# Performance work log

Hardware: AMD Instinct MI355X
Metric: run time of the kernel (lower is better)

Reference implementation:

```python
import jax, jax.numpy as jnp
import numpy as np

B, N, P, E, H, D, F, L = 16, 500, 100, 128, 8, 16, 512, 6
CLIP = 10.0  # logit_clipping


def _heads(x, h):
    b, n, _ = x.shape
    return x.reshape(b, n, h, -1).transpose(0, 2, 1, 3)  # [b,h,n,d]


def _mha(q, k, v, mask3=None):
    d = q.shape[-1]
    s = jnp.einsum('bhnd,bhmd->bhnm', q, k) / jnp.sqrt(jnp.asarray(d, q.dtype))
    if mask3 is not None:
        s = s + mask3[:, None, :, :]
    w = jax.nn.softmax(s, axis=-1)
    o = jnp.einsum('bhnm,bhmd->bhnd', w, v)
    b, h, n, dd = o.shape
    return o.transpose(0, 2, 1, 3).reshape(b, n, h * dd)


def _ff(x, w1, b1, w2, b2):
    return jax.nn.relu(x @ w1 + b1) @ w2 + b2


def _forward(depot_xy, node_xy, node_demand, load, cur_dist, ninf_mask,
             emb_depot_w, emb_depot_b, emb_node_w, emb_node_b,
             enc_wq, enc_wk, enc_wv, enc_comb_w, enc_comb_b,
             enc_ff1_w, enc_ff1_b, enc_ff2_w, enc_ff2_b,
             dec_wq_last, dec_wk, dec_wv, dec_comb_w, dec_comb_b,
             dec_cap_w, dec_ff1_w, dec_ff1_b, dec_ff2_w, dec_ff2_b,
             current_node):
    # ---------------- encoder ----------------
    node_xy_demand = jnp.concatenate([node_xy, node_demand[:, :, None]], axis=2)  # [B,N,3]
    x = jnp.concatenate([depot_xy @ emb_depot_w + emb_depot_b,
                         node_xy_demand @ emb_node_w + emb_node_b], axis=1)  # [B,N+1,E]
    for i in range(L):
        q = _heads(x @ enc_wq[i], H)
        k = _heads(x @ enc_wk[i], H)
        v = _heads(x @ enc_wv[i], H)
        mh = _mha(q, k, v) @ enc_comb_w[i] + enc_comb_b[i]
        o1 = x + mh
        x = o1 + _ff(o1, enc_ff1_w[i], enc_ff1_b[i], enc_ff2_w[i], enc_ff2_b[i])
    encoded_nodes = x  # [B, N+1, E]
    # decoder kv cache (set_kv)
    k = _heads(encoded_nodes @ dec_wk, H)
    v = _heads(encoded_nodes @ dec_wv, H)
    # ---------------- one decode step ----------------
    encoded_last = jnp.take_along_axis(encoded_nodes, current_node[:, :, None], axis=1)  # [B,P,E]
    input_cat = jnp.concatenate([encoded_last, load[:, :, None]], axis=2)  # [B,P,E+1]
    q = _heads(input_cat @ dec_wq_last, H)
    mh = _mha(q, k, v, mask3=ninf_mask) @ dec_comb_w + dec_comb_b
    mh = mh + encoded_last + load[:, :, None] @ dec_cap_w
    q_ref = _ff(mh, dec_ff1_w, dec_ff1_b, dec_ff2_w, dec_ff2_b) + mh
    score = jnp.einsum('bpe,bne->bpn', q_ref, encoded_nodes) / jnp.sqrt(jnp.asarray(E, q_ref.dtype))
    # distance-based noise injection
    dmin = cur_dist.min(axis=-1, keepdims=True)
    dmax = cur_dist.max(axis=-1, keepdims=True)
    norm_dist = (cur_dist - dmin) / (dmax - dmin + 1e-6)
    problem_size = ninf_mask.shape[2]
    nm = 50.0 / problem_size
    base_noise = jax.random.normal(jax.random.key(42), cur_dist.shape, cur_dist.dtype) * 0.2 + 0.5
    score = score - (1.0 - nm) * jnp.log(norm_dist + 1e-6) + base_noise * nm
    score = CLIP * jnp.tanh(score) + ninf_mask
    return jax.nn.softmax(score, axis=2)  # [B,P,N+1]


def setup_inputs() -> dict:
    key = jax.random.key(0)
    ks = iter(jax.random.split(key, 40))
    def rn(shape, s=0.02):
        return s * jax.random.normal(next(ks), shape, jnp.float32)
    return dict(
        depot_xy=jax.random.uniform(next(ks), (B, 1, 2), jnp.float32),
        node_xy=jax.random.uniform(next(ks), (B, N, 2), jnp.float32),
        node_demand=jax.random.uniform(next(ks), (B, N), jnp.float32),
        load=jax.random.uniform(next(ks), (B, P), jnp.float32),
        cur_dist=jax.random.uniform(next(ks), (B, P, N + 1), jnp.float32),
        ninf_mask=jnp.zeros((B, P, N + 1), jnp.float32),
        current_node=jax.random.randint(next(ks), (B, P), 0, N + 1),
        emb_depot_w=rn((2, E)), emb_depot_b=rn((E,)),
        emb_node_w=rn((3, E)), emb_node_b=rn((E,)),
        enc_wq=rn((L, E, H * D)), enc_wk=rn((L, E, H * D)), enc_wv=rn((L, E, H * D)),
        enc_comb_w=rn((L, H * D, E)), enc_comb_b=rn((L, E)),
        enc_ff1_w=rn((L, E, F)), enc_ff1_b=rn((L, F)),
        enc_ff2_w=rn((L, F, E)), enc_ff2_b=rn((L, E)),
        dec_wq_last=rn((E + 1, H * D)), dec_wk=rn((E, H * D)), dec_wv=rn((E, H * D)),
        dec_comb_w=rn((H * D, E)), dec_comb_b=rn((E,)),
        dec_cap_w=rn((1, E)),
        dec_ff1_w=rn((E, F)), dec_ff1_b=rn((F,)),
        dec_ff2_w=rn((F, E)), dec_ff2_b=rn((E,)),
    )


def reference(depot_xy, node_xy, node_demand, load, cur_dist, ninf_mask, current_node,
              emb_depot_w, emb_depot_b, emb_node_w, emb_node_b,
              enc_wq, enc_wk, enc_wv, enc_comb_w, enc_comb_b,
              enc_ff1_w, enc_ff1_b, enc_ff2_w, enc_ff2_b,
              dec_wq_last, dec_wk, dec_wv, dec_comb_w, dec_comb_b,
              dec_cap_w, dec_ff1_w, dec_ff1_b, dec_ff2_w, dec_ff2_b):
    return _forward(depot_xy, node_xy, node_demand, load, cur_dist, ninf_mask,
                    emb_depot_w, emb_depot_b, emb_node_w, emb_node_b,
                    enc_wq, enc_wk, enc_wv, enc_comb_w, enc_comb_b,
                    enc_ff1_w, enc_ff1_b, enc_ff2_w, enc_ff2_b,
                    dec_wq_last, dec_wk, dec_wv, dec_comb_w, dec_comb_b,
                    dec_cap_w, dec_ff1_w, dec_ff1_b, dec_ff2_w, dec_ff2_b,
                    current_node)
```

## Files before the change

### kernel.cpp

```cpp
#include <hip/hip_runtime.h>
#include <math.h>

#define Bb 16
#define Nn 500
#define NT 501
#define Pp 100
#define Ee 128
#define Hh 8
#define Dd 16
#define Ff 512
#define Ll 6
#define Mtok (Bb*NT)
#define PR (Bb*Pp)
#define TJ 32
#define SPLIT 4
#define KSEG 126
#define DSPLIT 4
#define DSEG 126
#define ENCP (6*128*384)
#define DECP (128*256)
#define SNP 512

__global__ __launch_bounds__(256) void pack_k(
    const float* __restrict__ ewq, const float* __restrict__ ewk, const float* __restrict__ ewv,
    const float* __restrict__ dwk, const float* __restrict__ dwv,
    float* __restrict__ encP, float* __restrict__ decP)
{
  int i = blockIdx.x*256 + threadIdx.x;
  if (i < ENCP) {
    int l = i / (128*384); int rem = i - l*128*384; int k = rem / 384; int n = rem - k*384;
    float v;
    if (n < 128)      v = ewq[((size_t)l*128 + k)*128 + n];
    else if (n < 256) v = ewk[((size_t)l*128 + k)*128 + (n-128)];
    else              v = ewv[((size_t)l*128 + k)*128 + (n-256)];
    encP[i] = v;
  } else {
    int j = i - ENCP;
    if (j < DECP) {
      int k = j >> 8; int n = j & 255;
      decP[j] = (n < 128) ? dwk[k*128 + n] : dwv[k*128 + (n-128)];
    }
  }
}

__global__ __launch_bounds__(256) void embed_k(
    const float* __restrict__ depot_xy, const float* __restrict__ node_xy,
    const float* __restrict__ node_demand,
    const float* __restrict__ wD, const float* __restrict__ bD,
    const float* __restrict__ wN, const float* __restrict__ bN,
    float* __restrict__ x)
{
  int t = blockIdx.x*256 + threadIdx.x;
  if (t >= Mtok*Ee) return;
  int e   = t & (Ee-1);
  int tok = t >> 7;
  int b   = tok / NT;
  int n   = tok - b*NT;
  float v;
  if (n == 0) {
    v = depot_xy[b*2+0]*wD[0*Ee+e] + depot_xy[b*2+1]*wD[1*Ee+e] + bD[e];
  } else {
    int nn = n - 1;
    float c0 = node_xy[(b*Nn + nn)*2 + 0];
    float c1 = node_xy[(b*Nn + nn)*2 + 1];
    float c2 = node_demand[b*Nn + nn];
    v = c0*wN[0*Ee+e] + c1*wN[1*Ee+e] + c2*wN[2*Ee+e] + bN[e];
  }
  x[(size_t)tok*Ee + e] = v;
}

__global__ __launch_bounds__(256) void gemm_k(
    const float* __restrict__ A, const float* __restrict__ W,
    const float* __restrict__ bias, const float* __restrict__ res,
    float* __restrict__ C, int M, int N, int K, int relu)
{
  __shared__ __align__(16) float As[2][16][68];
  __shared__ __align__(16) float Bs[2][16][68];
  int tid = threadIdx.x;
  int tx = tid & 15, ty = tid >> 4;
  int m0 = blockIdx.x * 64, n0 = blockIdx.y * 64;
  float acc[4][4];
  #pragma unroll
  for (int i=0;i<4;i++)
    #pragma unroll
    for (int j=0;j<4;j++) acc[i][j] = 0.f;

  int ar = tid >> 2;
  int ak = (tid & 3) << 2;
  int br = tid >> 4;
  int bc = (tid & 15) << 2;

  const float* Ap = A + (size_t)(m0 + ar)*K + ak;
  const float* Wp = W + (size_t)br*N + n0 + bc;
  bool aok = (m0 + ar) < M;

  float4 av = aok ? *(const float4*)(Ap) : make_float4(0.f,0.f,0.f,0.f);
  float4 wv = *(const float4*)(Wp);

  int nk = K >> 4;
  for (int t = 0; t < nk; ++t) {
    int cur = t & 1;
    As[cur][ak+0][ar] = av.x; As[cur][ak+1][ar] = av.y;
    As[cur][ak+2][ar] = av.z; As[cur][ak+3][ar] = av.w;
    *(float4*)(&Bs[cur][br][bc]) = wv;
    __syncthreads();
    if (t+1 < nk) {
      av = aok ? *(const float4*)(Ap + (t+1)*16) : make_float4(0.f,0.f,0.f,0.f);
      wv = *(const float4*)(Wp + (size_t)(t+1)*16*N);
    }
    #pragma unroll
    for (int k=0;k<16;k++){
      float4 a4 = *(const float4*)(&As[cur][k][ty*4]);
      float4 b4 = *(const float4*)(&Bs[cur][k][tx*4]);
      float avv[4] = {a4.x,a4.y,a4.z,a4.w};
      float bvv[4] = {b4.x,b4.y,b4.z,b4.w};
      #pragma unroll
      for (int i=0;i<4;i++)
        #pragma unroll
        for (int j=0;j<4;j++)
          acc[i][j] = fmaf(avv[i], bvv[j], acc[i][j]);
    }
  }

  float4 bv = make_float4(0.f,0.f,0.f,0.f);
  if (bias) bv = *(const float4*)(bias + n0 + tx*4);
  #pragma unroll
  for (int i=0;i<4;i++){
    int row = m0 + ty*4 + i;
    if (row >= M) continue;
    float4 o;
    o.x = acc[i][0] + bv.x; o.y = acc[i][1] + bv.y;
    o.z = acc[i][2] + bv.z; o.w = acc[i][3] + bv.w;
    if (relu){ o.x=fmaxf(o.x,0.f); o.y=fmaxf(o.y,0.f); o.z=fmaxf(o.z,0.f); o.w=fmaxf(o.w,0.f); }
    if (res){
      float4 rv = *(const float4*)(res + (size_t)row*N + n0 + tx*4);
      o.x += rv.x; o.y += rv.y; o.z += rv.z; o.w += rv.w;
    }
    *(float4*)(C + (size_t)row*N + n0 + tx*4) = o;
  }
}

__device__ __forceinline__ float dot4(float4 a, float4 b){
  return fmaf(a.x,b.x, fmaf(a.y,b.y, fmaf(a.z,b.z, a.w*b.w)));
}

__global__ __launch_bounds__(256) void attn_enc_k(
    const float* __restrict__ QKV, float* __restrict__ part_o,
    float* __restrict__ part_l)
{
  int blk = blockIdx.x;
  int s  = blk % SPLIT;
  int cc = blk / SPLIT;
  int c  = cc & 1;
  int bh = cc >> 1;
  int h  = bh & (Hh-1);
  int b  = bh >> 3;
  int p  = c*256 + (int)threadIdx.x;
  const int klo = s*KSEG;
  int kseg = NT - klo; if (kseg > KSEG) kseg = KSEG;

  __shared__ __align__(16) float4 Ks[2][TJ][4];
  __shared__ __align__(16) float4 Vs[2][TJ][4];

  int tid = threadIdx.x;
  int row = (tid >> 2) & 31;
  int lc  = tid & 3;
  bool isV = tid >= 128;
  const int kvoff = isV ? 256 : 128;

  float4 q0,q1,q2,q3;
  if (p < NT) {
    const float4* qp = (const float4*)(QKV + ((size_t)(b*NT + p))*384 + h*Dd);
    q0=qp[0]; q1=qp[1]; q2=qp[2]; q3=qp[3];
  } else {
    q0=q1=q2=q3=make_float4(0,0,0,0);
  }

  if (row < kseg) {
    float4 v = *((const float4*)(QKV + ((size_t)(b*NT + klo + row))*384 + kvoff + h*Dd) + lc);
    if (isV) Vs[0][row][lc] = v; else Ks[0][row][lc] = v;
  }
  __syncthreads();

  float l = 0.f;
  float4 o0=make_float4(0,0,0,0), o1=o0, o2=o0, o3=o0;
  const int ntiles = (kseg + TJ - 1)/TJ;
  int buf = 0;

  for (int t = 0; t < ntiles; ++t) {
    int j0 = t*TJ;
    if (t+1 < ntiles) {
      int jj = j0 + TJ + row;
      if (jj < kseg) {
        float4 v = *((const float4*)(QKV + ((size_t)(b*NT + klo + jj))*384 + kvoff + h*Dd) + lc);
        if (isV) Vs[buf^1][row][lc] = v; else Ks[buf^1][row][lc] = v;
      }
    }
    int jend = kseg - j0; if (jend > TJ) jend = TJ;

    if (p < NT) {
      #pragma unroll 4
      for (int jj=0;jj<jend;jj++){
        const float4* kr = &Ks[buf][jj][0];
        float s0 = (dot4(q0,kr[0])+dot4(q1,kr[1])) + (dot4(q2,kr[2])+dot4(q3,kr[3]));
        float w = __expf(s0 * 0.25f);
        l += w;
        const float4* vr = &Vs[buf][jj][0];
        float4 v0=vr[0],v1=vr[1],v2=vr[2],v3=vr[3];
        o0.x=fmaf(w,v0.x,o0.x); o0.y=fmaf(w,v0.y,o0.y); o0.z=fmaf(w,v0.z,o0.z); o0.w=fmaf(w,v0.w,o0.w);
        o1.x=fmaf(w,v1.x,o1.x); o1.y=fmaf(w,v1.y,o1.y); o1.z=fmaf(w,v1.z,o1.z); o1.w=fmaf(w,v1.w,o1.w);
        o2.x=fmaf(w,v2.x,o2.x); o2.y=fmaf(w,v2.y,o2.y); o2.z=fmaf(w,v2.z,o2.z); o2.w=fmaf(w,v2.w,o2.w);
        o3.x=fmaf(w,v3.x,o3.x); o3.y=fmaf(w,v3.y,o3.y); o3.z=fmaf(w,v3.z,o3.z); o3.w=fmaf(w,v3.w,o3.w);
      }
    }
    __syncthreads();
    buf ^= 1;
  }

  if (p < NT) {
    size_t rbase = ((size_t)s*128 + bh)*NT + p;
    float4* po = (float4*)(part_o + rbase*16);
    po[0]=o0; po[1]=o1; po[2]=o2; po[3]=o3;
    part_l[rbase] = l;
  }
}

__global__ __launch_bounds__(256) void attn_comb_k(
    const float* __restrict__ part_o, const float* __restrict__ part_l,
    float* __restrict__ O)
{
  int t = blockIdx.x*256 + threadIdx.x;
  if (t >= 128*NT*16) return;
  int d  = t & 15;
  int rq = t >> 4;
  int q  = rq % NT;
  int bh = rq / NT;
  int h = bh & 7, b = bh >> 3;
  const size_t R = (size_t)128*NT;
  float L = 0.f, o = 0.f;
  #pragma unroll
  for (int s=0;s<SPLIT;s++){
    L += part_l[(size_t)s*R + rq];
    o += part_o[((size_t)s*R + rq)*16 + d];
  }
  O[((size_t)(b*NT + q))*Ee + h*Dd + d] = o / L;
}

__global__ __launch_bounds__(128) void attn_dec_k(
    const float* __restrict__ Q, const float* __restrict__ KV,
    const float* __restrict__ mask,
    float* __restrict__ part_o, float* __restrict__ part_l)
{
  int blk = blockIdx.x;
  int s  = blk & (DSPLIT-1);
  int bh = blk >> 2;
  int h  = bh & (Hh-1);
  int b  = bh >> 3;
  int klo = s*DSEG;
  int kn  = NT - klo; if (kn > DSEG) kn = DSEG;

  __shared__ __align__(16) float4 Ks[DSEG][4];
  __shared__ __align__(16) float4 Vs[DSEG][4];

  int tid = threadIdx.x;
  for (int i = tid; i < kn*8; i += 128) {
    int row  = i >> 3;
    int q8   = i & 7;
    int quad = q8 & 3;
    int isv  = q8 >> 2;
    float4 v = *(const float4*)(KV + ((size_t)(b*NT + klo + row))*256 + isv*128 + h*Dd + quad*4);
    if (isv) Vs[row][quad] = v; else Ks[row][quad] = v;
  }
  __syncthreads();

  int p = tid;
  if (p >= Pp) return;
  int r = b*Pp + p;
  const float4* qp = (const float4*)(Q + (size_t)r*Ee + h*Dd);
  float4 qa=qp[0], qb=qp[1], qc=qp[2], qd=qp[3];
  const float* mrow = mask + (size_t)r*NT + klo;

  float l = 0.f;
  float4 o0=make_float4(0,0,0,0), o1=o0, o2=o0, o3=o0;
  for (int j=0;j<kn;++j){
    float sc = (dot4(qa,Ks[j][0])+dot4(qb,Ks[j][1])) + (dot4(qc,Ks[j][2])+dot4(qd,Ks[j][3]));
    float w = __expf(sc*0.25f + mrow[j]);
    l += w;
    float4 v0=Vs[j][0],v1=Vs[j][1],v2=Vs[j][2],v3=Vs[j][3];
    o0.x=fmaf(w,v0.x,o0.x); o0.y=fmaf(w,v0.y,o0.y); o0.z=fmaf(w,v0.z,o0.z); o0.w=fmaf(w,v0.w,o0.w);
    o1.x=fmaf(w,v1.x,o1.x); o1.y=fmaf(w,v1.y,o1.y); o1.z=fmaf(w,v1.z,o1.z); o1.w=fmaf(w,v1.w,o1.w);
    o2.x=fmaf(w,v2.x,o2.x); o2.y=fmaf(w,v2.y,o2.y); o2.z=fmaf(w,v2.z,o2.z); o2.w=fmaf(w,v2.w,o2.w);
    o3.x=fmaf(w,v3.x,o3.x); o3.y=fmaf(w,v3.y,o3.y); o3.z=fmaf(w,v3.z,o3.z); o3.w=fmaf(w,v3.w,o3.w);
  }

  size_t rb = ((size_t)s*PR + r)*Hh + h;
  float4* po = (float4*)(part_o + rb*16);
  po[0]=o0; po[1]=o1; po[2]=o2; po[3]=o3;
  part_l[rb] = l;
}

__global__ __launch_bounds__(256) void attn_dcomb_k(
    const float* __restrict__ part_o, const float* __restrict__ part_l,
    float* __restrict__ O)
{
  int t = blockIdx.x*256 + threadIdx.x;
  if (t >= PR*Ee) return;
  int d = t & 15;
  int h = (t >> 4) & 7;
  int r = t >> 7;
  const size_t S = (size_t)PR*Hh;
  size_t rb = (size_t)r*Hh + h;
  float L = 0.f, o = 0.f;
  #pragma unroll
  for (int s=0;s<DSPLIT;s++){
    L += part_l[(size_t)s*S + rb];
    o += part_o[((size_t)s*S + rb)*16 + d];
  }
  O[(size_t)r*Ee + h*Dd + d] = o / L;
}

__global__ __launch_bounds__(256) void gather_k(
    const float* __restrict__ x, const int* __restrict__ cur, float* __restrict__ encl)
{
  int t = blockIdx.x*256 + threadIdx.x;
  if (t >= PR*Ee) return;
  int e = t & (Ee-1);
  int r = t >> 7;
  int b = r / Pp;
  int node = cur[r];
  encl[(size_t)r*Ee + e] = x[((size_t)(b*NT + node))*Ee + e];
}

__global__ __launch_bounds__(128) void decq_k(
    const float* __restrict__ encl, const float* __restrict__ loadv,
    const float* __restrict__ Wq, float* __restrict__ q)
{
  __shared__ float row[Ee];
  int r = blockIdx.x, e = threadIdx.x;
  row[e] = encl[(size_t)r*Ee + e];
  __syncthreads();
  float acc = 0.f;
  #pragma unroll 4
  for (int k=0;k<Ee;k++) acc = fmaf(row[k], Wq[k*128 + e], acc);
  acc = fmaf(loadv[r], Wq[Ee*128 + e], acc);
  q[(size_t)r*128 + e] = acc;
}

__global__ __launch_bounds__(128) void dec_comb_k(
    const float* __restrict__ att, const float* __restrict__ W,
    const float* __restrict__ bias, const float* __restrict__ encl,
    const float* __restrict__ loadv, const float* __restrict__ capw,
    float* __restrict__ mh)
{
  __shared__ float row[Ee];
  int r = blockIdx.x, e = threadIdx.x;
  row[e] = att[(size_t)r*Ee + e];
  __syncthreads();
  float acc = 0.f;
  #pragma unroll 4
  for (int k=0;k<Ee;k++) acc = fmaf(row[k], W[k*Ee + e], acc);
  mh[(size_t)r*Ee + e] = acc + bias[e] + encl[(size_t)r*Ee + e] + loadv[r]*capw[e];
}

__global__ __launch_bounds__(256) void xt_k(
    const float* __restrict__ x, float* __restrict__ xT)
{
  __shared__ float T[32][33];
  int n0 = blockIdx.x * 32;
  int k0 = blockIdx.y * 32;
  int b  = blockIdx.z;
  int t  = threadIdx.x;
  int row = t >> 3;
  int c4  = (t & 7) << 2;

  int n = n0 + row;
  float4 v = make_float4(0.f,0.f,0.f,0.f);
  if (n < NT) v = *(const float4*)(x + ((size_t)(b*NT + n))*Ee + k0 + c4);
  T[c4+0][row] = v.x; T[c4+1][row] = v.y; T[c4+2][row] = v.z; T[c4+3][row] = v.w;
  __syncthreads();

  const float SC = 0.08838834764831845f;
  float4 o;
  o.x = T[row][c4+0]*SC; o.y = T[row][c4+1]*SC;
  o.z = T[row][c4+2]*SC; o.w = T[row][c4+3]*SC;
  *(float4*)(xT + ((size_t)(b*Ee + k0 + row))*SNP + n0 + c4) = o;
}

__global__ __launch_bounds__(256) void score_gemm_k(
    const float* __restrict__ qref, const float* __restrict__ xT,
    float* __restrict__ score)
{
  __shared__ __align__(16) float As[2][16][68];
  __shared__ __align__(16) float Bs[2][16][68];
  int tid = threadIdx.x;
  int tx = tid & 15, ty = tid >> 4;
  int m0 = blockIdx.x * 64;
  int n0 = blockIdx.y * 64;
  int b  = blockIdx.z;

  const float* A = qref + (size_t)b*Pp*Ee;
  const float* W = xT   + (size_t)b*Ee*SNP;
  float*       C = score + (size_t)b*Pp*SNP;

  float acc[4][4];
  #pragma unroll
  for (int i=0;i<4;i++)
    #pragma unroll
    for (int j=0;j<4;j++) acc[i][j] = 0.f;

  int ar = tid >> 2;
  int ak = (tid & 3) << 2;
  int br = tid >> 4;
  int bc = (tid & 15) << 2;

  const float* Ap = A + (size_t)(m0 + ar)*Ee + ak;
  const float* Wp = W + (size_t)br*SNP + n0 + bc;
  bool aok = (m0 + ar) < Pp;

  float4 av = aok ? *(const float4*)(Ap) : make_float4(0.f,0.f,0.f,0.f);
  float4 wv = *(const float4*)(Wp);

  for (int t = 0; t < 8; ++t) {
    int cur = t & 1;
    As[cur][ak+0][ar] = av.x; As[cur][ak+1][ar] = av.y;
    As[cur][ak+2][ar] = av.z; As[cur][ak+3][ar] = av.w;
    *(float4*)(&Bs[cur][br][bc]) = wv;
    __syncthreads();
    if (t+1 < 8) {
      av = aok ? *(const float4*)(Ap + (t+1)*16) : make_float4(0.f,0.f,0.f,0.f);
      wv = *(const float4*)(Wp + (size_t)(t+1)*16*SNP);
    }
    #pragma unroll
    for (int k=0;k<16;k++){
      float4 a4 = *(const float4*)(&As[cur][k][ty*4]);
      float4 b4 = *(const float4*)(&Bs[cur][k][tx*4]);
      float avv[4] = {a4.x,a4.y,a4.z,a4.w};
      float bvv[4] = {b4.x,b4.y,b4.z,b4.w};
      #pragma unroll
      for (int i=0;i<4;i++)
        #pragma unroll
        for (int j=0;j<4;j++)
          acc[i][j] = fmaf(avv[i], bvv[j], acc[i][j]);
    }
    __syncthreads();
  }

  #pragma unroll
  for (int i=0;i<4;i++){
    int row = m0 + ty*4 + i;
    if (row >= Pp) continue;
    float4 o;
    o.x = acc[i][0]; o.y = acc[i][1]; o.z = acc[i][2]; o.w = acc[i][3];
    *(float4*)(C + (size_t)row*SNP + n0 + tx*4) = o;
  }
}

__device__ __forceinline__ unsigned rotl32(unsigned x, int r){ return (x<<r)|(x>>(32-r)); }

__device__ float tf_normal(unsigned idx)
{
  unsigned x0 = 0u;
  unsigned x1 = idx;
  const unsigned ks[3] = {0u, 42u, 0u ^ 42u ^ 0x1BD11BDAu};
  x0 += ks[0]; x1 += ks[1];
  const int rotA[4] = {13,15,26,6};
  const int rotB[4] = {17,29,16,24};
  #pragma unroll
  for (int i=0;i<5;i++){
    #pragma unroll
    for (int q=0;q<4;q++){
      int rr = (i&1) ? rotB[q] : rotA[q];
      x0 += x1; x1 = rotl32(x1, rr); x1 ^= x0;
    }
    x0 += ks[(i+1)%3];
    x1 += ks[(i+2)%3] + (unsigned)(i+1);
  }
  unsigned bits = x0 ^ x1;
  float f = __uint_as_float((bits >> 9) | 0x3f800000u) - 1.0f;
  const float lo = -0.99999994f;
  float u = f * 2.0f + lo;
  u = fmaxf(lo, u);
  float w = -log1pf(-u*u);
  float p;
  if (w < 5.0f) {
    w -= 2.5f;
    p = 2.81022636e-08f;
    p = fmaf(p, w, 3.43273939e-07f);
    p = fmaf(p, w, -3.5233877e-06f);
    p = fmaf(p, w, -4.39150654e-06f);
    p = fmaf(p, w, 0.00021858087f);
    p = fmaf(p, w, -0.00125372503f);
    p = fmaf(p, w, -0.00417768164f);
    p = fmaf(p, w, 0.246640727f);
    p = fmaf(p, w, 1.50140941f);
  } else {
    w = sqrtf(w) - 3.0f;
    p = -0.000200214257f;
    p = fmaf(p, w, 0.000100950558f);
    p = fmaf(p, w, 0.00134934322f);
    p = fmaf(p, w, -0.00367342844f);
    p = fmaf(p, w, 0.00573950773f);
    p = fmaf(p, w, -0.0076224613f);
    p = fmaf(p, w, 0.00943887047f);
    p = fmaf(p, w, 1.00167406f);
    p = fmaf(p, w, 2.83297682f);
  }
  return 1.4142135623730951f * (p * u);
}

__global__ __launch_bounds__(512) void final_k(
    const float* __restrict__ score, const float* __restrict__ cur_dist,
    const float* __restrict__ ninf, float* __restrict__ out)
{
  __shared__ float smn[8], smx[8], sm2[8], ss[8];
  const float NM = (float)(50.0/501.0);
  const float C1 = (float)(1.0 - 50.0/501.0);
  int r = blockIdx.x;
  int t = threadIdx.x;
  int wid = t >> 6, lane = t & 63;

  float cd = 0.f;
  float mn = 1e30f, mx = -1e30f;
  if (t < NT) { cd = cur_dist[(size_t)r*NT + t]; mn = cd; mx = cd; }
  #pragma unroll
  for (int off=32; off>=1; off>>=1){
    mn = fminf(mn, __shfl_xor(mn, off));
    mx = fmaxf(mx, __shfl_xor(mx, off));
  }
  if (lane == 0){ smn[wid] = mn; smx[wid] = mx; }
  __syncthreads();
  float dmin = smn[0], dmax = smx[0];
  #pragma unroll
  for (int i=1;i<8;i++){ dmin = fminf(dmin, smn[i]); dmax = fmaxf(dmax, smx[i]); }

  float sval = -1e30f;
  if (t < NT) {
    float nd = (cd - dmin) / (dmax - dmin + 1e-6f);
    float z  = tf_normal((unsigned)r*501u + (unsigned)t);
    float s  = score[(size_t)r*SNP + t] - C1*logf(nd + 1e-6f) + (z*0.2f + 0.5f)*NM;
    sval = 10.0f*tanhf(s) + ninf[(size_t)r*NT + t];
  }
  float mv = sval;
  #pragma unroll
  for (int off=32; off>=1; off>>=1) mv = fmaxf(mv, __shfl_xor(mv, off));
  if (lane == 0) sm2[wid] = mv;
  __syncthreads();
  float smax = sm2[0];
  #pragma unroll
  for (int i=1;i<8;i++) smax = fmaxf(smax, sm2[i]);

  float e = (t < NT) ? expf(sval - smax) : 0.f;
  float sv = e;
  #pragma unroll
  for (int off=32; off>=1; off>>=1) sv += __shfl_xor(sv, off);
  if (lane == 0) ss[wid] = sv;
  __syncthreads();
  float ssum = ss[0];
  #pragma unroll
  for (int i=1;i<8;i++) ssum += ss[i];

  if (t < NT) out[(size_t)r*NT + t] = e / ssum;
}

extern "C" void kernel_launch(void* const* d_in, const int* in_sizes, int n_in,
                              void* d_out, int out_size, void* d_ws, size_t ws_size,
                              hipStream_t stream)
{
  (void)in_sizes; (void)n_in; (void)out_size; (void)ws_size;
  const float* depot_xy    = (const float*)d_in[0];
  const float* node_xy     = (const float*)d_in[1];
  const float* node_demand = (const float*)d_in[2];
  const float* loadv       = (const float*)d_in[3];
  const float* cur_dist    = (const float*)d_in[4];
  const float* ninf        = (const float*)d_in[5];
  const int*   cur_node    = (const int*)d_in[6];
  const float* emb_depot_w = (const float*)d_in[7];
  const float* emb_depot_b = (const float*)d_in[8];
  const float* emb_node_w  = (const float*)d_in[9];
  const float* emb_node_b  = (const float*)d_in[10];
  const float* enc_wq      = (const float*)d_in[11];
  const float* enc_wk      = (const float*)d_in[12];
  const float* enc_wv      = (const float*)d_in[13];
  const float* enc_comb_w  = (const float*)d_in[14];
  const float* enc_comb_b  = (const float*)d_in[15];
  const float* enc_ff1_w   = (const float*)d_in[16];
  const float* enc_ff1_b   = (const float*)d_in[17];
  const float* enc_ff2_w   = (const float*)d_in[18];
  const float* enc_ff2_b   = (const float*)d_in[19];
  const float* dec_wq_last = (const float*)d_in[20];
  const float* dec_wk      = (const float*)d_in[21];
  const float* dec_wv      = (const float*)d_in[22];
  const float* dec_comb_w  = (const float*)d_in[23];
  const float* dec_comb_b  = (const float*)d_in[24];
  const float* dec_cap_w   = (const float*)d_in[25];
  const float* dec_ff1_w   = (const float*)d_in[26];
  const float* dec_ff1_b   = (const float*)d_in[27];
  const float* dec_ff2_w   = (const float*)d_in[28];
  const float* dec_ff2_b   = (const float*)d_in[29];

  float* ws = (float*)d_ws;
  const size_t SZ = (size_t)Mtok*Ee;
  float* xb    = ws + 0*SZ;
  float* qkvb  = ws + 1*SZ;
  float* atb   = ws + 4*SZ;
  float* o1b   = ws + 5*SZ;
  float* ffb   = ws + 6*SZ;
  float* encPk = ws + 10*SZ;
  float* decPk = encPk + ENCP;
  float* part_o = ffb;
  float* part_l = o1b;
  float* dpart_o = ffb;
  float* dpart_l = o1b;
  float* encl  = qkvb + 2*SZ;
  float* qdec  = encl + 204800;
  float* attd  = qdec + 204800;
  float* mhb   = attd + 204800;
  float* qrefb = atb;
  float* ffh2  = ffb;
  float* xTb   = ffb;
  float* scoreb= o1b;

  pack_k<<<(ENCP + DECP + 255)/256, 256, 0, stream>>>(
      enc_wq, enc_wk, enc_wv, dec_wk, dec_wv, encPk, decPk);

  embed_k<<<(Mtok*Ee + 255)/256, 256, 0, stream>>>(
      depot_xy, node_xy, node_demand, emb_depot_w, emb_depot_b,
      emb_node_w, emb_node_b, xb);

  dim3 gqkv((Mtok + 63)/64, 384/64);
  dim3 g128((Mtok + 63)/64, Ee/64);
  dim3 gff ((Mtok + 63)/64, Ff/64);
  const int gcomb = (128*NT*16 + 255)/256;
  for (int l = 0; l < Ll; ++l) {
    gemm_k<<<gqkv, 256, 0, stream>>>(xb, encPk + (size_t)l*128*384, nullptr, nullptr, qkvb, Mtok, 384, Ee, 0);
    attn_enc_k<<<Bb*Hh*2*SPLIT, 256, 0, stream>>>(qkvb, part_o, part_l);
    attn_comb_k<<<gcomb, 256, 0, stream>>>(part_o, part_l, atb);
    gemm_k<<<g128, 256, 0, stream>>>(atb, enc_comb_w + (size_t)l*Ee*Ee, enc_comb_b + l*Ee, xb, o1b, Mtok, Ee, Ee, 0);
    gemm_k<<<gff, 256, 0, stream>>>(o1b, enc_ff1_w + (size_t)l*Ee*Ff, enc_ff1_b + l*Ff, nullptr, ffb, Mtok, Ff, Ee, 1);
    gemm_k<<<g128, 256, 0, stream>>>(ffb, enc_ff2_w + (size_t)l*Ff*Ee, enc_ff2_b + l*Ee, o1b, xb, Mtok, Ee, Ff, 0);
  }

  dim3 gkv((Mtok + 63)/64, 256/64);
  gemm_k<<<gkv, 256, 0, stream>>>(xb, decPk, nullptr, nullptr, qkvb, Mtok, 256, Ee, 0);
  gather_k<<<(PR*Ee + 255)/256, 256, 0, stream>>>(xb, cur_node, encl);
  decq_k<<<PR, 128, 0, stream>>>(encl, loadv, dec_wq_last, qdec);
  attn_dec_k<<<Bb*Hh*DSPLIT, 128, 0, stream>>>(qdec, qkvb, ninf, dpart_o, dpart_l);
  attn_dcomb_k<<<(PR*Ee + 255)/256, 256, 0, stream>>>(dpart_o, dpart_l, attd);
  dec_comb_k<<<PR, 128, 0, stream>>>(attd, dec_comb_w, dec_comb_b, encl, loadv, dec_cap_w, mhb);
  dim3 gd1((PR + 63)/64, Ff/64);
  gemm_k<<<gd1, 256, 0, stream>>>(mhb, dec_ff1_w, dec_ff1_b, nullptr, ffh2, PR, Ff, Ee, 1);
  dim3 gd2((PR + 63)/64, Ee/64);
  gemm_k<<<gd2, 256, 0, stream>>>(ffh2, dec_ff2_w, dec_ff2_b, mhb, qrefb, PR, Ee, Ff, 0);
  dim3 gxt(16, 4, 16);
  xt_k<<<gxt, 256, 0, stream>>>(xb, xTb);
  dim3 gsc(2, 8, 16);
  score_gemm_k<<<gsc, 256, 0, stream>>>(qrefb, xTb, scoreb);
  final_k<<<PR, 512, 0, stream>>>(scoreb, cur_dist, ninf, (float*)d_out);
}
```

Before: 909.5 us.

## Fuse attention split-combine into projection GEMMs and retile attention kernels

The encoder split-K attention combine is folded into the output-projection GEMM, which reads the partial sums directly, and the attention kernel now uses 128 threads that each handle two queries so K/V loads from shared memory are reused. In the decoder, the gather is merged into the query projection and the partial combine into the comb-projection kernel. The decoder split count also goes from 4 to 16 for more parallelism. This removes several launches and intermediate round trips, at the cost of redundant partial reads inside the GEMM and more registers in the attention kernel.

```diff
diff --git a/kernel.cpp b/kernel.cpp
--- a/kernel.cpp
+++ b/kernel.cpp
@@ -15,8 +15,8 @@
 #define TJ 32
 #define SPLIT 4
 #define KSEG 126
-#define DSPLIT 4
-#define DSEG 126
+#define DSPLIT 16
+#define DSEG 32
 #define ENCP (6*128*384)
 #define DECP (128*256)
 #define SNP 512
@@ -144,7 +144,7 @@
   return fmaf(a.x,b.x, fmaf(a.y,b.y, fmaf(a.z,b.z, a.w*b.w)));
 }
 
-__global__ __launch_bounds__(256) void attn_enc_k(
+__global__ __launch_bounds__(128) void attn_enc_k(
     const float* __restrict__ QKV, float* __restrict__ part_o,
     float* __restrict__ part_l)
 {
@@ -155,95 +155,172 @@
   int bh = cc >> 1;
   int h  = bh & (Hh-1);
   int b  = bh >> 3;
-  int p  = c*256 + (int)threadIdx.x;
+  int tid = threadIdx.x;
+  int p0 = c*256 + tid;
+  int p1 = p0 + 128;
   const int klo = s*KSEG;
   int kseg = NT - klo; if (kseg > KSEG) kseg = KSEG;
 
   __shared__ __align__(16) float4 Ks[2][TJ][4];
   __shared__ __align__(16) float4 Vs[2][TJ][4];
 
-  int tid = threadIdx.x;
-  int row = (tid >> 2) & 31;
-  int lc  = tid & 3;
-  bool isV = tid >= 128;
-  const int kvoff = isV ? 256 : 128;
-
-  float4 q0,q1,q2,q3;
-  if (p < NT) {
-    const float4* qp = (const float4*)(QKV + ((size_t)(b*NT + p))*384 + h*Dd);
-    q0=qp[0]; q1=qp[1]; q2=qp[2]; q3=qp[3];
+  bool vbq = p1 < NT;
+
+  const float4* qp = (const float4*)(QKV + ((size_t)(b*NT + p0))*384 + h*Dd);
+  float4 qa0=qp[0], qa1=qp[1], qa2=qp[2], qa3=qp[3];
+  float4 qb0,qb1,qb2,qb3;
+  if (vbq) {
+    const float4* q2 = (const float4*)(QKV + ((size_t)(b*NT + p1))*384 + h*Dd);
+    qb0=q2[0]; qb1=q2[1]; qb2=q2[2]; qb3=q2[3];
   } else {
-    q0=q1=q2=q3=make_float4(0,0,0,0);
-  }
-
-  if (row < kseg) {
-    float4 v = *((const float4*)(QKV + ((size_t)(b*NT + klo + row))*384 + kvoff + h*Dd) + lc);
-    if (isV) Vs[0][row][lc] = v; else Ks[0][row][lc] = v;
+    qb0=qb1=qb2=qb3=make_float4(0,0,0,0);
+  }
+
+  {
+    int rows = kseg < TJ ? kseg : TJ;
+    for (int i = tid; i < rows*8; i += 128) {
+      int row = i >> 3; int q8 = i & 7; int quad = q8 & 3; int isv = q8 >> 2;
+      float4 v = *(const float4*)(QKV + ((size_t)(b*NT + klo + row))*384 + (isv ? 256 : 128) + h*Dd + quad*4);
+      if (isv) Vs[0][row][quad] = v; else Ks[0][row][quad] = v;
+    }
   }
   __syncthreads();
 
-  float l = 0.f;
-  float4 o0=make_float4(0,0,0,0), o1=o0, o2=o0, o3=o0;
+  float lA = 0.f, lB = 0.f;
+  float4 oA0=make_float4(0,0,0,0), oA1=oA0, oA2=oA0, oA3=oA0;
+  float4 oB0=oA0, oB1=oA0, oB2=oA0, oB3=oA0;
   const int ntiles = (kseg + TJ - 1)/TJ;
   int buf = 0;
 
   for (int t = 0; t < ntiles; ++t) {
     int j0 = t*TJ;
     if (t+1 < ntiles) {
-      int jj = j0 + TJ + row;
-      if (jj < kseg) {
-        float4 v = *((const float4*)(QKV + ((size_t)(b*NT + klo + jj))*384 + kvoff + h*Dd) + lc);
-        if (isV) Vs[buf^1][row][lc] = v; else Ks[buf^1][row][lc] = v;
+      int j1 = j0 + TJ;
+      int rows = kseg - j1; if (rows > TJ) rows = TJ;
+      for (int i = tid; i < rows*8; i += 128) {
+        int row = i >> 3; int q8 = i & 7; int quad = q8 & 3; int isv = q8 >> 2;
+        float4 v = *(const float4*)(QKV + ((size_t)(b*NT + klo + j1 + row))*384 + (isv ? 256 : 128) + h*Dd + quad*4);
+        if (isv) Vs[buf^1][row][quad] = v; else Ks[buf^1][row][quad] = v;
       }
     }
     int jend = kseg - j0; if (jend > TJ) jend = TJ;
 
-    if (p < NT) {
-      #pragma unroll 4
-      for (int jj=0;jj<jend;jj++){
-        const float4* kr = &Ks[buf][jj][0];
-        float s0 = (dot4(q0,kr[0])+dot4(q1,kr[1])) + (dot4(q2,kr[2])+dot4(q3,kr[3]));
-        float w = __expf(s0 * 0.25f);
-        l += w;
-        const float4* vr = &Vs[buf][jj][0];
-        float4 v0=vr[0],v1=vr[1],v2=vr[2],v3=vr[3];
-        o0.x=fmaf(w,v0.x,o0.x); o0.y=fmaf(w,v0.y,o0.y); o0.z=fmaf(w,v0.z,o0.z); o0.w=fmaf(w,v0.w,o0.w);
-        o1.x=fmaf(w,v1.x,o1.x); o1.y=fmaf(w,v1.y,o1.y); o1.z=fmaf(w,v1.z,o1.z); o1.w=fmaf(w,v1.w,o1.w);
-        o2.x=fmaf(w,v2.x,o2.x); o2.y=fmaf(w,v2.y,o2.y); o2.z=fmaf(w,v2.z,o2.z); o2.w=fmaf(w,v2.w,o2.w);
-        o3.x=fmaf(w,v3.x,o3.x); o3.y=fmaf(w,v3.y,o3.y); o3.z=fmaf(w,v3.z,o3.z); o3.w=fmaf(w,v3.w,o3.w);
-      }
+    #pragma unroll 2
+    for (int jj = 0; jj < jend; ++jj) {
+      float4 k0=Ks[buf][jj][0], k1=Ks[buf][jj][1], k2=Ks[buf][jj][2], k3=Ks[buf][jj][3];
+      float sA = (dot4(qa0,k0)+dot4(qa1,k1)) + (dot4(qa2,k2)+dot4(qa3,k3));
+      float sB = (dot4(qb0,k0)+dot4(qb1,k1)) + (dot4(qb2,k2)+dot4(qb3,k3));
+      float wA = __expf(sA*0.25f);
+      float wB = __expf(sB*0.25f);
+      lA += wA; lB += wB;
+      float4 v0=Vs[buf][jj][0], v1=Vs[buf][jj][1], v2=Vs[buf][jj][2], v3=Vs[buf][jj][3];
+      oA0.x=fmaf(wA,v0.x,oA0.x); oA0.y=fmaf(wA,v0.y,oA0.y); oA0.z=fmaf(wA,v0.z,oA0.z); oA0.w=fmaf(wA,v0.w,oA0.w);
+      oA1.x=fmaf(wA,v1.x,oA1.x); oA1.y=fmaf(wA,v1.y,oA1.y); oA1.z=fmaf(wA,v1.z,oA1.z); oA1.w=fmaf(wA,v1.w,oA1.w);
+      oA2.x=fmaf(wA,v2.x,oA2.x); oA2.y=fmaf(wA,v2.y,oA2.y); oA2.z=fmaf(wA,v2.z,oA2.z); oA2.w=fmaf(wA,v2.w,oA2.w);
+      oA3.x=fmaf(wA,v3.x,oA3.x); oA3.y=fmaf(wA,v3.y,oA3.y); oA3.z=fmaf(wA,v3.z,oA3.z); oA3.w=fmaf(wA,v3.w,oA3.w);
+      oB0.x=fmaf(wB,v0.x,oB0.x); oB0.y=fmaf(wB,v0.y,oB0.y); oB0.z=fmaf(wB,v0.z,oB0.z); oB0.w=fmaf(wB,v0.w,oB0.w);
+      oB1.x=fmaf(wB,v1.x,oB1.x); oB1.y=fmaf(wB,v1.y,oB1.y); oB1.z=fmaf(wB,v1.z,oB1.z); oB1.w=fmaf(wB,v1.w,oB1.w);
+      oB2.x=fmaf(wB,v2.x,oB2.x); oB2.y=fmaf(wB,v2.y,oB2.y); oB2.z=fmaf(wB,v2.z,oB2.z); oB2.w=fmaf(wB,v2.w,oB2.w);
+      oB3.x=fmaf(wB,v3.x,oB3.x); oB3.y=fmaf(wB,v3.y,oB3.y); oB3.z=fmaf(wB,v3.z,oB3.z); oB3.w=fmaf(wB,v3.w,oB3.w);
     }
     __syncthreads();
     buf ^= 1;
   }
 
-  if (p < NT) {
-    size_t rbase = ((size_t)s*128 + bh)*NT + p;
-    float4* po = (float4*)(part_o + rbase*16);
-    po[0]=o0; po[1]=o1; po[2]=o2; po[3]=o3;
-    part_l[rbase] = l;
-  }
-}
-
-__global__ __launch_bounds__(256) void attn_comb_k(
+  size_t r0 = ((size_t)s*128 + bh)*NT + p0;
+  float4* po0 = (float4*)(part_o + r0*16);
+  po0[0]=oA0; po0[1]=oA1; po0[2]=oA2; po0[3]=oA3;
+  part_l[r0] = lA;
+  if (vbq) {
+    size_t r1 = ((size_t)s*128 + bh)*NT + p1;
+    float4* po1 = (float4*)(part_o + r1*16);
+    po1[0]=oB0; po1[1]=oB1; po1[2]=oB2; po1[3]=oB3;
+    part_l[r1] = lB;
+  }
+}
+
+__global__ __launch_bounds__(256) void comb_gemm_k(
     const float* __restrict__ part_o, const float* __restrict__ part_l,
-    float* __restrict__ O)
-{
-  int t = blockIdx.x*256 + threadIdx.x;
-  if (t >= 128*NT*16) return;
-  int d  = t & 15;
-  int rq = t >> 4;
-  int q  = rq % NT;
-  int bh = rq / NT;
-  int h = bh & 7, b = bh >> 3;
-  const size_t R = (size_t)128*NT;
-  float L = 0.f, o = 0.f;
-  #pragma unroll
-  for (int s=0;s<SPLIT;s++){
-    L += part_l[(size_t)s*R + rq];
-    o += part_o[((size_t)s*R + rq)*16 + d];
-  }
-  O[((size_t)(b*NT + q))*Ee + h*Dd + d] = o / L;
+    const float* __restrict__ W, const float* __restrict__ bias,
+    const float* __restrict__ res, float* __restrict__ C)
+{
+  __shared__ __align__(16) float As[2][16][68];
+  __shared__ __align__(16) float Bs[2][16][68];
+  int tid = threadIdx.x;
+  int tx = tid & 15, ty = tid >> 4;
+  int m0 = blockIdx.x * 64, n0 = blockIdx.y * 64;
+  float acc[4][4];
+  #pragma unroll
+  for (int i=0;i<4;i++)
+    #pragma unroll
+    for (int j=0;j<4;j++) acc[i][j] = 0.f;
+
+  int ar = tid >> 2;
+  int ak = (tid & 3) << 2;
+  int br = tid >> 4;
+  int bc = (tid & 15) << 2;
+
+  int row = m0 + ar;
+  bool aok = row < Mtok;
+  int tok = aok ? row : 0;
+  int bb = tok / NT;
+  int p  = tok - bb*NT;
+  const size_t pbase = ((size_t)(bb*8))*NT + p;
+
+  const float* Wp = W + (size_t)br*Ee + n0 + bc;
+
+  #define LOADA(t, dst) { \
+    float4 o4 = make_float4(0.f,0.f,0.f,0.f); float l = 0.f; \
+    _Pragma("unroll") \
+    for (int s=0;s<SPLIT;s++){ \
+      size_t idx = (size_t)s*((size_t)128*NT) + pbase + (size_t)(t)*NT; \
+      float4 v = *(const float4*)(part_o + idx*16 + ak); \
+      o4.x+=v.x; o4.y+=v.y; o4.z+=v.z; o4.w+=v.w; \
+      l += part_l[idx]; \
+    } \
+    float inv = aok ? 1.f/l : 0.f; \
+    dst = make_float4(o4.x*inv, o4.y*inv, o4.z*inv, o4.w*inv); \
+  }
+
+  float4 av; LOADA(0, av);
+  float4 wv = *(const float4*)(Wp);
+
+  for (int t = 0; t < 8; ++t) {
+    int cur = t & 1;
+    As[cur][ak+0][ar] = av.x; As[cur][ak+1][ar] = av.y;
+    As[cur][ak+2][ar] = av.z; As[cur][ak+3][ar] = av.w;
+    *(float4*)(&Bs[cur][br][bc]) = wv;
+    __syncthreads();
+    if (t+1 < 8) {
+      LOADA(t+1, av);
+      wv = *(const float4*)(Wp + (size_t)(t+1)*16*Ee);
+    }
+    #pragma unroll
+    for (int k=0;k<16;k++){
+      float4 a4 = *(const float4*)(&As[cur][k][ty*4]);
+      float4 b4 = *(const float4*)(&Bs[cur][k][tx*4]);
+      float avv[4] = {a4.x,a4.y,a4.z,a4.w};
+      float bvv[4] = {b4.x,b4.y,b4.z,b4.w};
+      #pragma unroll
+      for (int i=0;i<4;i++)
+        #pragma unroll
+        for (int j=0;j<4;j++)
+          acc[i][j] = fmaf(avv[i], bvv[j], acc[i][j]);
+    }
+  }
+  #undef LOADA
+
+  float4 bv = *(const float4*)(bias + n0 + tx*4);
+  #pragma unroll
+  for (int i=0;i<4;i++){
+    int orow = m0 + ty*4 + i;
+    if (orow >= Mtok) continue;
+    float4 o;
+    float4 rv = *(const float4*)(res + (size_t)orow*Ee + n0 + tx*4);
+    o.x = acc[i][0] + bv.x + rv.x; o.y = acc[i][1] + bv.y + rv.y;
+    o.z = acc[i][2] + bv.z + rv.z; o.w = acc[i][3] + bv.w + rv.w;
+    *(float4*)(C + (size_t)orow*Ee + n0 + tx*4) = o;
+  }
 }
 
 __global__ __launch_bounds__(128) void attn_dec_k(
@@ -253,7 +330,7 @@
 {
   int blk = blockIdx.x;
   int s  = blk & (DSPLIT-1);
-  int bh = blk >> 2;
+  int bh = blk >> 4;
   int h  = bh & (Hh-1);
   int b  = bh >> 3;
   int klo = s*DSEG;
@@ -299,45 +376,18 @@
   part_l[rb] = l;
 }
 
-__global__ __launch_bounds__(256) void attn_dcomb_k(
-    const float* __restrict__ part_o, const float* __restrict__ part_l,
-    float* __restrict__ O)
-{
-  int t = blockIdx.x*256 + threadIdx.x;
-  if (t >= PR*Ee) return;
-  int d = t & 15;
-  int h = (t >> 4) & 7;
-  int r = t >> 7;
-  const size_t S = (size_t)PR*Hh;
-  size_t rb = (size_t)r*Hh + h;
-  float L = 0.f, o = 0.f;
-  #pragma unroll
-  for (int s=0;s<DSPLIT;s++){
-    L += part_l[(size_t)s*S + rb];
-    o += part_o[((size_t)s*S + rb)*16 + d];
-  }
-  O[(size_t)r*Ee + h*Dd + d] = o / L;
-}
-
-__global__ __launch_bounds__(256) void gather_k(
-    const float* __restrict__ x, const int* __restrict__ cur, float* __restrict__ encl)
-{
-  int t = blockIdx.x*256 + threadIdx.x;
-  if (t >= PR*Ee) return;
-  int e = t & (Ee-1);
-  int r = t >> 7;
+__global__ __launch_bounds__(128) void decq_k(
+    const float* __restrict__ x, const int* __restrict__ cur,
+    const float* __restrict__ loadv, const float* __restrict__ Wq,
+    float* __restrict__ q, float* __restrict__ encl)
+{
+  __shared__ float row[Ee];
+  int r = blockIdx.x, e = threadIdx.x;
   int b = r / Pp;
   int node = cur[r];
-  encl[(size_t)r*Ee + e] = x[((size_t)(b*NT + node))*Ee + e];
-}
-
-__global__ __launch_bounds__(128) void decq_k(
-    const float* __restrict__ encl, const float* __restrict__ loadv,
-    const float* __restrict__ Wq, float* __restrict__ q)
-{
-  __shared__ float row[Ee];
-  int r = blockIdx.x, e = threadIdx.x;
-  row[e] = encl[(size_t)r*Ee + e];
+  float xv = x[((size_t)(b*NT + node))*Ee + e];
+  encl[(size_t)r*Ee + e] = xv;
+  row[e] = xv;
   __syncthreads();
   float acc = 0.f;
   #pragma unroll 4
@@ -347,14 +397,23 @@
 }
 
 __global__ __launch_bounds__(128) void dec_comb_k(
-    const float* __restrict__ att, const float* __restrict__ W,
-    const float* __restrict__ bias, const float* __restrict__ encl,
-    const float* __restrict__ loadv, const float* __restrict__ capw,
-    float* __restrict__ mh)
+    const float* __restrict__ dpart_o, const float* __restrict__ dpart_l,
+    const float* __restrict__ W, const float* __restrict__ bias,
+    const float* __restrict__ encl, const float* __restrict__ loadv,
+    const float* __restrict__ capw, float* __restrict__ mh)
 {
   __shared__ float row[Ee];
   int r = blockIdx.x, e = threadIdx.x;
-  row[e] = att[(size_t)r*Ee + e];
+  int h = e >> 4, d = e & 15;
+  const size_t S = (size_t)PR*Hh;
+  size_t rb = (size_t)r*Hh + h;
+  float L = 0.f, o = 0.f;
+  #pragma unroll
+  for (int s=0;s<DSPLIT;s++){
+    L += dpart_l[(size_t)s*S + rb];
+    o += dpart_o[((size_t)s*S + rb)*16 + d];
+  }
+  row[e] = o / L;
   __syncthreads();
   float acc = 0.f;
   #pragma unroll 4
@@ -607,14 +666,13 @@
   float* ffb   = ws + 6*SZ;
   float* encPk = ws + 10*SZ;
   float* decPk = encPk + ENCP;
-  float* part_o = ffb;
-  float* part_l = o1b;
+  float* part_o  = ffb;
+  float* epart_l = atb;
   float* dpart_o = ffb;
   float* dpart_l = o1b;
   float* encl  = qkvb + 2*SZ;
   float* qdec  = encl + 204800;
-  float* attd  = qdec + 204800;
-  float* mhb   = attd + 204800;
+  float* mhb   = qdec + 204800;
   float* qrefb = atb;
   float* ffh2  = ffb;
   float* xTb   = ffb;
@@ -628,25 +686,23 @@
       emb_node_w, emb_node_b, xb);
 
   dim3 gqkv((Mtok + 63)/64, 384/64);
+  dim3 gcombg((Mtok + 63)/64, Ee/64);
+  dim3 gff ((Mtok + 63)/64, Ff/64);
   dim3 g128((Mtok + 63)/64, Ee/64);
-  dim3 gff ((Mtok + 63)/64, Ff/64);
-  const int gcomb = (128*NT*16 + 255)/256;
   for (int l = 0; l < Ll; ++l) {
     gemm_k<<<gqkv, 256, 0, stream>>>(xb, encPk + (size_t)l*128*384, nullptr, nullptr, qkvb, Mtok, 384, Ee, 0);
-    attn_enc_k<<<Bb*Hh*2*SPLIT, 256, 0, stream>>>(qkvb, part_o, part_l);
-    attn_comb_k<<<gcomb, 256, 0, stream>>>(part_o, part_l, atb);
-    gemm_k<<<g128, 256, 0, stream>>>(atb, enc_comb_w + (size_t)l*Ee*Ee, enc_comb_b + l*Ee, xb, o1b, Mtok, Ee, Ee, 0);
+    attn_enc_k<<<Bb*Hh*2*SPLIT, 128, 0, stream>>>(qkvb, part_o, epart_l);
+    comb_gemm_k<<<gcombg, 256, 0, stream>>>(part_o, epart_l, enc_comb_w + (size_t)l*Ee*Ee,
+                                            enc_comb_b + l*Ee, xb, o1b);
     gemm_k<<<gff, 256, 0, stream>>>(o1b, enc_ff1_w + (size_t)l*Ee*Ff, enc_ff1_b + l*Ff, nullptr, ffb, Mtok, Ff, Ee, 1);
     gemm_k<<<g128, 256, 0, stream>>>(ffb, enc_ff2_w + (size_t)l*Ff*Ee, enc_ff2_b + l*Ee, o1b, xb, Mtok, Ee, Ff, 0);
   }
 
   dim3 gkv((Mtok + 63)/64, 256/64);
   gemm_k<<<gkv, 256, 0, stream>>>(xb, decPk, nullptr, nullptr, qkvb, Mtok, 256, Ee, 0);
-  gather_k<<<(PR*Ee + 255)/256, 256, 0, stream>>>(xb, cur_node, encl);
-  decq_k<<<PR, 128, 0, stream>>>(encl, loadv, dec_wq_last, qdec);
+  decq_k<<<PR, 128, 0, stream>>>(xb, cur_node, loadv, dec_wq_last, qdec, encl);
   attn_dec_k<<<Bb*Hh*DSPLIT, 128, 0, stream>>>(qdec, qkvb, ninf, dpart_o, dpart_l);
-  attn_dcomb_k<<<(PR*Ee + 255)/256, 256, 0, stream>>>(dpart_o, dpart_l, attd);
-  dec_comb_k<<<PR, 128, 0, stream>>>(attd, dec_comb_w, dec_comb_b, encl, loadv, dec_cap_w, mhb);
+  dec_comb_k<<<PR, 128, 0, stream>>>(dpart_o, dpart_l, dec_comb_w, dec_comb_b, encl, loadv, dec_cap_w, mhb);
   dim3 gd1((PR + 63)/64, Ff/64);
   gemm_k<<<gd1, 256, 0, stream>>>(mhb, dec_ff1_w, dec_ff1_b, nullptr, ffh2, PR, Ff, Ee, 1);
   dim3 gd2((PR + 63)/64, Ee/64);
```

New measurement: 954.9 us. +5.0%, slower.
